# Performance work log

Hardware: AMD Instinct MI355X
Metric: run time of the kernel (lower is better)

The kernel has to match this reference:

```python
import jax, jax.numpy as jnp
import numpy as np

V, E, IN, OUT, K, NREL = 50000, 640000, 128, 128, 4, 237
D = IN // K   # 32
OD = OUT // K # 32

def setup_inputs() -> dict:
    key = jax.random.key(0)
    ks = jax.random.split(key, 20)
    s = 0.05
    return {
        'node_repr': jax.random.normal(ks[0], (V, IN), jnp.float32),
        'rel_repr': jax.random.normal(ks[1], (2 * NREL, IN), jnp.float32),
        'src': jax.random.randint(ks[2], (E,), 0, V, jnp.int32),
        'dst': jax.random.randint(ks[3], (E,), 0, V, jnp.int32),
        'etype': jax.random.randint(ks[4], (E,), 0, 2 * NREL, jnp.int32),
        'norm': jax.random.uniform(ks[5], (E,), jnp.float32),
        'node_w': jax.random.normal(ks[6], (K, IN, D), jnp.float32) * s,
        'node_rel_w': jax.random.normal(ks[7], (K, IN, D), jnp.float32) * s,
        'in_w': jax.random.normal(ks[8], (K, D, OD), jnp.float32) * s,
        'out_w': jax.random.normal(ks[9], (K, D, OD), jnp.float32) * s,
        'att_w': jax.random.normal(ks[10], (2 * D, 1), jnp.float32) * s,
        'loop_rel': jax.random.normal(ks[11], (1, IN), jnp.float32) * s,
        'loop_w': jax.random.normal(ks[12], (IN, OUT), jnp.float32) * s,
        'w_rel': jax.random.normal(ks[13], (IN, OUT), jnp.float32) * s,
        'bias': jnp.zeros((OUT,), jnp.float32),
        'bn_gamma': jnp.ones((OUT,), jnp.float32),
        'bn_beta': jnp.zeros((OUT,), jnp.float32),
    }

def reference(node_repr, rel_repr, src, dst, etype, norm,
              node_w, node_rel_w, in_w, out_w, att_w,
              loop_rel, loop_w, w_rel, bias, bn_gamma, bn_beta):
    e = E
    half = e // 2
    rel = rel_repr  # no bases
    # per-edge composition (opn='mult'): src feature * relation feature
    edge_comp = node_repr[src] * rel[etype]                      # [E, IN]
    edge_data = jnp.einsum('ei,kid->ekd', edge_comp, node_rel_w)  # [E, K, D]
    node_data = jnp.einsum('ei,kid->ekd', node_repr[dst], node_w) # [E, K, D]
    cat = jnp.concatenate([edge_data, node_data], axis=-1)       # [E, K, 2D]
    att = jax.nn.relu(cat @ att_w)                               # [E, K, 1]
    att = jax.nn.softmax(att, axis=1)                            # softmax over K factors
    edge_data = edge_data * att                                  # broadcast over D
    # factorized projection: first half edges -> in_w, second half -> out_w
    msg_in = jnp.einsum('ekd,kdo->eko', edge_data[:half], in_w)
    msg_out = jnp.einsum('ekd,kdo->eko', edge_data[half:], out_w)
    msg = jnp.concatenate([msg_in, msg_out], axis=0).reshape(e, OUT)
    msg = msg * norm[:, None]
    # scatter-sum into destination nodes, then /3 (drop_rate=0)
    h = jax.ops.segment_sum(msg, dst, num_segments=V) / 3.0      # [V, OUT]
    # self-loop term
    h = h + ((h * loop_rel) @ loop_w) / 3.0
    h = h + bias
    # BatchNorm1d (training-mode batch stats, biased variance, eps=1e-5)
    mean = jnp.mean(h, axis=0)
    var = jnp.var(h, axis=0)
    h = bn_gamma * (h - mean) * jax.lax.rsqrt(var + 1e-5) + bn_beta
    node_out = jnp.tanh(h)
    rel_out = rel @ w_rel
    return node_out, rel_out
```

## Files before the change

kernel.cpp:

```cpp
#include <hip/hip_runtime.h>

namespace {
constexpr int V = 50000;
constexpr int E = 640000;
constexpr int HALF = 320000;
constexpr int NREL2 = 474;
constexpr int C = 128;
constexpr int NCHUNK = (V + 255) / 256;
constexpr int NQBLK = V / 16;
constexpr int RELBLK = (NREL2 + 1) / 2;
}

typedef _Float16 h4 __attribute__((ext_vector_type(4)));
typedef _Float16 f16x8 __attribute__((ext_vector_type(8)));
typedef float f32x4 __attribute__((ext_vector_type(4)));

__global__ void prep_kernel(const float* __restrict__ nrw, const float* __restrict__ nw,
                            const float* __restrict__ inw, const float* __restrict__ outw,
                            const float* __restrict__ aw, const float* __restrict__ rel,
                            float* __restrict__ cbuf, float* __restrict__ bbuf,
                            _Float16* __restrict__ Mh, _Float16* __restrict__ rel_h) {
  int tid = blockIdx.x * 256 + threadIdx.x;
  if (tid < 512) {
    int k = tid >> 7, i = tid & 127;
    float acc = 0.f;
    for (int d = 0; d < 32; ++d) acc += nrw[k*4096 + i*32 + d] * aw[d];
    cbuf[tid] = acc;
  } else if (tid < 1024) {
    int u = tid - 512; int k = u >> 7, i = u & 127;
    float acc = 0.f;
    for (int d = 0; d < 32; ++d) acc += nw[k*4096 + i*32 + d] * aw[32 + d];
    bbuf[u] = acc;
  } else if (tid < 1024 + 16384) {
    int u = tid - 1024; int k = u >> 12, rem = u & 4095, i = rem >> 5, o = rem & 31;
    float acc = 0.f;
    for (int d = 0; d < 32; ++d) acc += nrw[k*4096 + i*32 + d] * inw[k*1024 + d*32 + o];
    Mh[(((k) * 2 + (o >> 4)) * 16 + (o & 15)) * 128 + i] = (_Float16)acc;
  } else if (tid < 1024 + 32768) {
    int u = tid - 1024 - 16384; int k = u >> 12, rem = u & 4095, i = rem >> 5, o = rem & 31;
    float acc = 0.f;
    for (int d = 0; d < 32; ++d) acc += nrw[k*4096 + i*32 + d] * outw[k*1024 + d*32 + o];
    Mh[(((4 + k) * 2 + (o >> 4)) * 16 + (o & 15)) * 128 + i] = (_Float16)acc;
  } else if (tid < 1024 + 32768 + NREL2 * C / 8) {
    int u = tid - 1024 - 32768;
    const float4 v0 = *(const float4*)(rel + (size_t)u * 8);
    const float4 v1 = *(const float4*)(rel + (size_t)u * 8 + 4);
    f16x8 o;
    o[0] = (_Float16)v0.x; o[1] = (_Float16)v0.y;
    o[2] = (_Float16)v0.z; o[3] = (_Float16)v0.w;
    o[4] = (_Float16)v1.x; o[5] = (_Float16)v1.y;
    o[6] = (_Float16)v1.z; o[7] = (_Float16)v1.w;
    *(f16x8*)(rel_h + (size_t)u * 8) = o;
  }
}

__global__ __launch_bounds__(256) void qnode_kernel(const float* __restrict__ nrp,
                                                    const float* __restrict__ bbuf,
                                                    float* __restrict__ qbuf,
                                                    _Float16* __restrict__ nrp_h,
                                                    const float* __restrict__ rel,
                                                    const float* __restrict__ wrel,
                                                    float* __restrict__ rel_out) {
  if (blockIdx.x >= NQBLK) {
    __shared__ float rr2[2][128];
    const int bb = blockIdx.x - NQBLK;
    const int half = threadIdx.x >> 7;
    const int t128 = threadIdx.x & 127;
    const int row = bb * 2 + half;
    if (row < NREL2) rr2[half][t128] = rel[row * C + t128];
    __syncthreads();
    if (row < NREL2) {
      float acc = 0.f;
#pragma unroll 4
      for (int i = 0; i < C; ++i) acc += rr2[half][i] * wrel[i * C + t128];
      rel_out[row * C + t128] = acc;
    }
    return;
  }
  const int t = blockIdx.x * 16 + (threadIdx.x >> 4);
  const int l = threadIdx.x & 15;
  if (t >= V) return;
  const float* row = nrp + (size_t)t * C + l * 8;
  float4 a0 = *(const float4*)(row);
  float4 a1 = *(const float4*)(row + 4);
  {
    f16x8 o;
    o[0] = (_Float16)a0.x; o[1] = (_Float16)a0.y;
    o[2] = (_Float16)a0.z; o[3] = (_Float16)a0.w;
    o[4] = (_Float16)a1.x; o[5] = (_Float16)a1.y;
    o[6] = (_Float16)a1.z; o[7] = (_Float16)a1.w;
    *(f16x8*)(nrp_h + (size_t)t * C + l * 8) = o;
  }
  float p[4];
#pragma unroll
  for (int k = 0; k < 4; ++k) {
    const float* brow = bbuf + k * C + l * 8;
    float4 b0 = *(const float4*)(brow);
    float4 b1 = *(const float4*)(brow + 4);
    p[k] = a0.x * b0.x + a0.y * b0.y + a0.z * b0.z + a0.w * b0.w
         + a1.x * b1.x + a1.y * b1.y + a1.z * b1.z + a1.w * b1.w;
  }
#pragma unroll
  for (int m = 1; m < 16; m <<= 1) {
#pragma unroll
    for (int k = 0; k < 4; ++k) p[k] += __shfl_xor(p[k], m);
  }
  if (l == 0) *(float4*)(qbuf + 4 * (size_t)t) = make_float4(p[0], p[1], p[2], p[3]);
}

__global__ void hist_kernel(const int* __restrict__ dst, int* __restrict__ cnt,
                            int* __restrict__ cin) {
  int e = blockIdx.x * 256 + threadIdx.x;
  if (e < E) {
    int t = dst[e];
    atomicAdd(&cnt[t], 1);
    if (e < HALF) atomicAdd(&cin[t], 1);
  }
}

__global__ void scan_sum_kernel(const int* __restrict__ cnt, int* __restrict__ bsum) {
  __shared__ int sd[256];
  int tid = threadIdx.x;
  int idx = blockIdx.x * 256 + tid;
  int v = (idx < V) ? cnt[idx] : 0;
  sd[tid] = v; __syncthreads();
  for (int s = 128; s > 0; s >>= 1) {
    if (tid < s) sd[tid] += sd[tid + s];
    __syncthreads();
  }
  if (tid == 0) bsum[blockIdx.x] = sd[0];
}

__global__ void scan_top_kernel(int* __restrict__ bsum) {
  __shared__ int sd[256];
  int tid = threadIdx.x;
  int v = (tid < NCHUNK) ? bsum[tid] : 0;
  sd[tid] = v; __syncthreads();
  for (int ofs = 1; ofs < 256; ofs <<= 1) {
    int t = (tid >= ofs) ? sd[tid - ofs] : 0;
    __syncthreads();
    sd[tid] += t;
    __syncthreads();
  }
  if (tid < NCHUNK) bsum[tid] = sd[tid] - v;
}

__global__ void scan_apply_kernel(const int* __restrict__ cnt, const int* __restrict__ cin,
                                  const int* __restrict__ bsum, int4* __restrict__ ninfo) {
  __shared__ int sd[256];
  int tid = threadIdx.x;
  int idx = blockIdx.x * 256 + tid;
  int v = (idx < V) ? cnt[idx] : 0;
  sd[tid] = v; __syncthreads();
  for (int ofs = 1; ofs < 256; ofs <<= 1) {
    int t = (tid >= ofs) ? sd[tid - ofs] : 0;
    __syncthreads();
    sd[tid] += t;
    __syncthreads();
  }
  if (idx < V) {
    int off = bsum[blockIdx.x] + sd[tid] - v;
    ninfo[idx] = make_int4(off, v, cin[idx], 0);
  }
}

__global__ void place_kernel(const int* __restrict__ dst, const int* __restrict__ src,
                             const int* __restrict__ etype, const float* __restrict__ norm,
                             const int4* __restrict__ ninfo,
                             int* __restrict__ cur_in, int* __restrict__ cur_out,
                             int2* __restrict__ em) {
  int e = blockIdx.x * 256 + threadIdx.x;
  if (e < E) {
    int t = dst[e];
    int off = ninfo[t].x;
    int pos;
    if (e < HALF) {
      pos = off + atomicAdd(&cur_in[t], 1);
    } else {
      pos = off + ninfo[t].z + atomicAdd(&cur_out[t], 1);
    }
    em[pos] = make_int2(src[e] | (etype[e] << 16), __float_as_int(norm[e]));
  }
}

__global__ __launch_bounds__(256) void fused_kernel(
    const _Float16* __restrict__ nrp_h, const _Float16* __restrict__ rel_h,
    const int4* __restrict__ ninfo, const float* __restrict__ qbuf,
    const float* __restrict__ cbuf, const int2* __restrict__ em,
    const _Float16* __restrict__ Mh, float* __restrict__ h) {
  __shared__ __align__(16) _Float16 z16[16384];
  const int w = threadIdx.x >> 6;
  const int lane = threadIdx.x & 63;
  const int dirg = lane >> 5;
  const int slot = (lane >> 4) & 1;
  const int ll = lane & 15;
  const int ch0 = ll * 8;

  float4 ckA[4], ckB[4];
#pragma unroll
  for (int k = 0; k < 4; ++k) {
    ckA[k] = *(const float4*)(cbuf + k * C + ch0);
    ckB[k] = *(const float4*)(cbuf + k * C + ch0 + 4);
  }

  for (int nn = 0; nn < 4; ++nn) {
    const int node = w * 4 + nn;
    const int t = blockIdx.x * 16 + node;
    const int4 nfo = ninfo[t];
    const int start = nfo.x, deg = nfo.y, ni = nfo.z;
    const float4 q4 = *(const float4*)(qbuf + 4 * (size_t)t);
    const int sidx = dirg ? ni : 0;
    const int nmy = dirg ? (deg - ni) : ni;
    const int nmax = max(ni, deg - ni);

    float4 zA[4], zB[4];
#pragma unroll
    for (int k = 0; k < 4; ++k) {
      zA[k] = make_float4(0.f, 0.f, 0.f, 0.f);
      zB[k] = make_float4(0.f, 0.f, 0.f, 0.f);
    }

    if (nmax > 0) {
      int2 em0 = em[start + min(sidx + slot, deg - 1)];
      int2 em1 = em[start + min(sidx + 2 + slot, deg - 1)];
      f16x8 ah = *(const f16x8*)(nrp_h + (size_t)(em0.x & 0xFFFF) * C + ch0);
      f16x8 bh = *(const f16x8*)(rel_h + (size_t)((em0.x >> 16) & 0x1FF) * C + ch0);

      for (int j = 0; j < nmax; j += 2) {
        int2 em2 = em1;
        if (j + 4 < nmax) em2 = em[start + min(sidx + j + 4 + slot, deg - 1)];
        f16x8 ahn = ah, bhn = bh;
        if (j + 2 < nmax) {
          ahn = *(const f16x8*)(nrp_h + (size_t)(em1.x & 0xFFFF) * C + ch0);
          bhn = *(const f16x8*)(rel_h + (size_t)((em1.x >> 16) & 0x1FF) * C + ch0);
        }
        float4 xA, xB;
        xA.x = (float)ah[0] * (float)bh[0];
        xA.y = (float)ah[1] * (float)bh[1];
        xA.z = (float)ah[2] * (float)bh[2];
        xA.w = (float)ah[3] * (float)bh[3];
        xB.x = (float)ah[4] * (float)bh[4];
        xB.y = (float)ah[5] * (float)bh[5];
        xB.z = (float)ah[6] * (float)bh[6];
        xB.w = (float)ah[7] * (float)bh[7];
        float p0 = xA.x * ckA[0].x + xA.y * ckA[0].y + xA.z * ckA[0].z + xA.w * ckA[0].w
                 + xB.x * ckB[0].x + xB.y * ckB[0].y + xB.z * ckB[0].z + xB.w * ckB[0].w;
        float p1 = xA.x * ckA[1].x + xA.y * ckA[1].y + xA.z * ckA[1].z + xA.w * ckA[1].w
                 + xB.x * ckB[1].x + xB.y * ckB[1].y + xB.z * ckB[1].z + xB.w * ckB[1].w;
        float p2 = xA.x * ckA[2].x + xA.y * ckA[2].y + xA.z * ckA[2].z + xA.w * ckA[2].w
                 + xB.x * ckB[2].x + xB.y * ckB[2].y + xB.z * ckB[2].z + xB.w * ckB[2].w;
        float p3 = xA.x * ckA[3].x + xA.y * ckA[3].y + xA.z * ckA[3].z + xA.w * ckA[3].w
                 + xB.x * ckB[3].x + xB.y * ckB[3].y + xB.z * ckB[3].z + xB.w * ckB[3].w;
#pragma unroll
        for (int m = 1; m < 16; m <<= 1) {
          p0 += __shfl_xor(p0, m);
          p1 += __shfl_xor(p1, m);
          p2 += __shfl_xor(p2, m);
          p3 += __shfl_xor(p3, m);
        }
        float l0 = fmaxf(p0 + q4.x, 0.f);
        float l1 = fmaxf(p1 + q4.y, 0.f);
        float l2 = fmaxf(p2 + q4.z, 0.f);
        float l3 = fmaxf(p3 + q4.w, 0.f);
        float e0f = __expf(l0), e1f = __expf(l1);
        float e2f = __expf(l2), e3f = __expf(l3);
        float nr = __int_as_float(em0.y);
        float inv = ((j + slot) < nmy) ? (nr / (e0f + e1f + e2f + e3f)) : 0.f;
        float w0 = e0f * inv, w1 = e1f * inv, w2 = e2f * inv, w3 = e3f * inv;
        zA[0].x += w0 * xA.x; zA[0].y += w0 * xA.y; zA[0].z += w0 * xA.z; zA[0].w += w0 * xA.w;
        zB[0].x += w0 * xB.x; zB[0].y += w0 * xB.y; zB[0].z += w0 * xB.z; zB[0].w += w0 * xB.w;
        zA[1].x += w1 * xA.x; zA[1].y += w1 * xA.y; zA[1].z += w1 * xA.z; zA[1].w += w1 * xA.w;
        zB[1].x += w1 * xB.x; zB[1].y += w1 * xB.y; zB[1].z += w1 * xB.z; zB[1].w += w1 * xB.w;
        zA[2].x += w2 * xA.x; zA[2].y += w2 * xA.y; zA[2].z += w2 * xA.z; zA[2].w += w2 * xA.w;
        zB[2].x += w2 * xB.x; zB[2].y += w2 * xB.y; zB[2].z += w2 * xB.z; zB[2].w += w2 * xB.w;
        zA[3].x += w3 * xA.x; zA[3].y += w3 * xA.y; zA[3].z += w3 * xA.z; zA[3].w += w3 * xA.w;
        zB[3].x += w3 * xB.x; zB[3].y += w3 * xB.y; zB[3].z += w3 * xB.z; zB[3].w += w3 * xB.w;
        em0 = em1; em1 = em2;
        ah = ahn; bh = bhn;
      }
    }

#pragma unroll
    for (int k = 0; k < 4; ++k) {
      zA[k].x += __shfl_xor(zA[k].x, 16);
      zA[k].y += __shfl_xor(zA[k].y, 16);
      zA[k].z += __shfl_xor(zA[k].z, 16);
      zA[k].w += __shfl_xor(zA[k].w, 16);
      zB[k].x += __shfl_xor(zB[k].x, 16);
      zB[k].y += __shfl_xor(zB[k].y, 16);
      zB[k].z += __shfl_xor(zB[k].z, 16);
      zB[k].w += __shfl_xor(zB[k].w, 16);
    }
    if (slot == 0) {
      const int swz = (node & 7) << 4;
      char* zb = (char*)z16 + node * 2048 + dirg * 1024 + ((ll * 16) ^ swz);
#pragma unroll
      for (int k = 0; k < 4; ++k) {
        f16x8 o;
        o[0] = (_Float16)zA[k].x; o[1] = (_Float16)zA[k].y;
        o[2] = (_Float16)zA[k].z; o[3] = (_Float16)zA[k].w;
        o[4] = (_Float16)zB[k].x; o[5] = (_Float16)zB[k].y;
        o[6] = (_Float16)zB[k].z; o[7] = (_Float16)zB[k].w;
        *(f16x8*)(zb + k * 256) = o;
      }
    }
  }
  __syncthreads();

  const int kk = w;
  const int lo16 = lane & 15;
  const int kq = lane >> 4;
  {
    const int anode = lo16;
    const int aswz = (anode & 7) << 4;
    const char* zb = (const char*)z16 + anode * 2048 + kk * 256;
    f16x8 a[2][4];
#pragma unroll
    for (int d = 0; d < 2; ++d)
#pragma unroll
      for (int kc = 0; kc < 4; ++kc)
        a[d][kc] = *(const f16x8*)(zb + d * 1024 + ((kc * 64 + kq * 16) ^ aswz));

    f32x4 c0 = {0.f, 0.f, 0.f, 0.f};
    f32x4 c1 = {0.f, 0.f, 0.f, 0.f};
#pragma unroll
    for (int d = 0; d < 2; ++d)
#pragma unroll
      for (int kc = 0; kc < 4; ++kc) {
        const _Float16* mb = Mh + (((d * 4 + kk) * 2) * 16 + lo16) * 128 + kc * 32 + kq * 8;
        f16x8 b0 = *(const f16x8*)(mb);
        f16x8 b1 = *(const f16x8*)(mb + 2048);
        c0 = __builtin_amdgcn_mfma_f32_16x16x32_f16(a[d][kc], b0, c0, 0, 0, 0);
        c1 = __builtin_amdgcn_mfma_f32_16x16x32_f16(a[d][kc], b1, c1, 0, 0, 0);
      }

    const float third = 1.f / 3.f;
#pragma unroll
    for (int r = 0; r < 4; ++r) {
      int tt = blockIdx.x * 16 + kq * 4 + r;
      if (tt < V) {
        size_t hb = (size_t)tt * C + kk * 32 + lo16;
        h[hb] = c0[r] * third;
        h[hb + 16] = c1[r] * third;
      }
    }
  }
}

__global__ __launch_bounds__(256, 4) void selfloop_kernel(
    float* __restrict__ h, const float* __restrict__ lr,
    const float* __restrict__ lw, const float* __restrict__ bias,
    float* __restrict__ bnsum, float* __restrict__ bnsq) {
  __shared__ float xr[4][8][128];
  __shared__ float red[256];
  const int tid = threadIdx.x;
  const int w = tid >> 6, lane = tid & 63;

  const int c0 = 2 * lane, c1 = c0 + 1;
  const float lr0 = lr[c0], lr1 = lr[c1];
  const float bv0 = bias[c0], bv1 = bias[c1];
  float s0 = 0.f, s1 = 0.f, sq0 = 0.f, sq1 = 0.f;

  const int wg = blockIdx.x * 4 + w;
  const int nw = gridDim.x * 4;
  for (int rb = wg * 8; rb < V; rb += nw * 8) {
    const int nrows = min(8, V - rb);
    float2 hv[8];
#pragma unroll
    for (int rr = 0; rr < 8; ++rr) {
      if (rr < nrows) {
        hv[rr] = *(const float2*)(h + (size_t)(rb + rr) * C + c0);
      } else {
        hv[rr] = make_float2(0.f, 0.f);
      }
      xr[w][rr][c0] = hv[rr].x * lr0;
      xr[w][rr][c1] = hv[rr].y * lr1;
    }
    float acc[8][2] = {};
    for (int i = 0; i < C; ++i) {
      float2 lwv = *(const float2*)(lw + i * C + c0);
#pragma unroll
      for (int rr = 0; rr < 8; ++rr) {
        float xv = xr[w][rr][i];
        acc[rr][0] += xv * lwv.x;
        acc[rr][1] += xv * lwv.y;
      }
    }
    const float third = 1.f / 3.f;
#pragma unroll
    for (int rr = 0; rr < 8; ++rr) {
      if (rr < nrows) {
        float h0 = hv[rr].x + acc[rr][0] * third + bv0;
        float h1 = hv[rr].y + acc[rr][1] * third + bv1;
        *(float2*)(h + (size_t)(rb + rr) * C + c0) = make_float2(h0, h1);
        s0 += h0; s1 += h1; sq0 += h0 * h0; sq1 += h1 * h1;
      }
    }
  }

  __syncthreads();
  red[tid] = s0; __syncthreads();
  if (tid < 64) {
    float v = red[tid] + red[tid + 64] + red[tid + 128] + red[tid + 192];
    atomicAdd(&bnsum[2 * tid], v);
  }
  __syncthreads();
  red[tid] = s1; __syncthreads();
  if (tid < 64) {
    float v = red[tid] + red[tid + 64] + red[tid + 128] + red[tid + 192];
    atomicAdd(&bnsum[2 * tid + 1], v);
  }
  __syncthreads();
  red[tid] = sq0; __syncthreads();
  if (tid < 64) {
    float v = red[tid] + red[tid + 64] + red[tid + 128] + red[tid + 192];
    atomicAdd(&bnsq[2 * tid], v);
  }
  __syncthreads();
  red[tid] = sq1; __syncthreads();
  if (tid < 64) {
    float v = red[tid] + red[tid + 64] + red[tid + 128] + red[tid + 192];
    atomicAdd(&bnsq[2 * tid + 1], v);
  }
}

__global__ void tanh_kernel(float* __restrict__ h,
                            const float* __restrict__ bnsum, const float* __restrict__ bnsq,
                            const float* __restrict__ gamma, const float* __restrict__ beta) {
  int idx = blockIdx.x * 256 + threadIdx.x;
  int base = idx * 4;
  if (base >= V * C) return;
  int j = base & 127;
  const float invV = 1.f / (float)V;
  float4 v = *(float4*)(h + base);
  float o[4] = {v.x, v.y, v.z, v.w};
#pragma unroll
  for (int cidx = 0; cidx < 4; ++cidx) {
    float mean = bnsum[j + cidx] * invV;
    float var = bnsq[j + cidx] * invV - mean * mean;
    float sc = gamma[j + cidx] * rsqrtf(var + 1e-5f);
    float sh = beta[j + cidx] - sc * mean;
    o[cidx] = tanhf(sc * o[cidx] + sh);
  }
  v.x = o[0]; v.y = o[1]; v.z = o[2]; v.w = o[3];
  *(float4*)(h + base) = v;
}

extern "C" void kernel_launch(void* const* d_in, const int* in_sizes, int n_in,
                              void* d_out, int out_size, void* d_ws, size_t ws_size,
                              hipStream_t stream) {
  const float* node_repr  = (const float*)d_in[0];
  const float* rel_repr   = (const float*)d_in[1];
  const int*   src        = (const int*)d_in[2];
  const int*   dst        = (const int*)d_in[3];
  const int*   etype      = (const int*)d_in[4];
  const float* norm       = (const float*)d_in[5];
  const float* node_w     = (const float*)d_in[6];
  const float* node_rel_w = (const float*)d_in[7];
  const float* in_w       = (const float*)d_in[8];
  const float* out_w      = (const float*)d_in[9];
  const float* att_w      = (const float*)d_in[10];
  const float* loop_rel   = (const float*)d_in[11];
  const float* loop_w     = (const float*)d_in[12];
  const float* w_rel      = (const float*)d_in[13];
  const float* bias       = (const float*)d_in[14];
  const float* bn_gamma   = (const float*)d_in[15];
  const float* bn_beta    = (const float*)d_in[16];

  float* out = (float*)d_out;
  float* h = out;
  float* rel_out = out + (size_t)V * C;

  int* cnt = (int*)d_ws;
  int* cur_in = cnt + V;
  int* cin = cur_in + V;
  int* cur_out = cin + V;
  float* bnsum = (float*)(cur_out + V);
  float* bnsq = bnsum + 128;
  int* bsum = (int*)(bnsq + 128);
  int4* ninfo = (int4*)(bsum + 256);
  int2* em = (int2*)(ninfo + V);
  float* qbuf = (float*)(em + E);
  float* cbuf = qbuf + 4 * V;
  float* bbuf = cbuf + 512;
  _Float16* Mh = (_Float16*)(bbuf + 512);
  _Float16* nrp_h = Mh + 32768;
  _Float16* rel_h = nrp_h + (size_t)V * C;

  hipMemsetAsync(cnt, 0, (size_t)(4 * V + 256) * 4, stream);

  prep_kernel<<<(1024 + 32768 + NREL2 * C / 8 + 255) / 256, 256, 0, stream>>>(
      node_rel_w, node_w, in_w, out_w, att_w, rel_repr, cbuf, bbuf, Mh, rel_h);
  qnode_kernel<<<NQBLK + RELBLK, 256, 0, stream>>>(node_repr, bbuf, qbuf, nrp_h,
                                                   rel_repr, w_rel, rel_out);
  hist_kernel<<<E / 256, 256, 0, stream>>>(dst, cnt, cin);
  scan_sum_kernel<<<NCHUNK, 256, 0, stream>>>(cnt, bsum);
  scan_top_kernel<<<1, 256, 0, stream>>>(bsum);
  scan_apply_kernel<<<NCHUNK, 256, 0, stream>>>(cnt, cin, bsum, ninfo);
  place_kernel<<<E / 256, 256, 0, stream>>>(dst, src, etype, norm, ninfo,
                                            cur_in, cur_out, em);
  fused_kernel<<<(V + 15) / 16, 256, 0, stream>>>(nrp_h, rel_h, ninfo,
                                                  qbuf, cbuf, em, Mh, h);
  selfloop_kernel<<<1024, 256, 0, stream>>>(h, loop_rel, loop_w, bias, bnsum, bnsq);
  tanh_kernel<<<(V * C / 4 + 255) / 256, 256, 0, stream>>>(h, bnsum, bnsq, bn_gamma, bn_beta);
}
```

Measured before the change: 319.2 us.

## Compute self-loop projection with fp16 MFMA using prefolded loop weight matrix

The self-loop GEMM (h*loop_rel)@loop_w/3 moves from a scalar FP32 FMA loop to 16x16x32 fp16 MFMA tiles. loop_rel and the 1/3 factor are folded into a transposed fp16 weight matrix in the prep kernel. Each block stages a 16-row tile of h as fp16 in swizzled shared memory, and the BN partial sums are reduced with wave shuffles instead of shared-memory rounds. The aim is to cut ALU time in this kernel, at the cost of fp16 rounding of h and of the weights in the self-loop term.

Result: faster. 270.2 us (-15.4%).

```diff
diff --git a/kernel.cpp b/kernel.cpp
--- a/kernel.cpp
+++ b/kernel.cpp
@@ -9,6 +9,7 @@
 constexpr int NCHUNK = (V + 255) / 256;
 constexpr int NQBLK = V / 16;
 constexpr int RELBLK = (NREL2 + 1) / 2;
+constexpr int NTILES = V / 16;
 }
 
 typedef _Float16 h4 __attribute__((ext_vector_type(4)));
@@ -18,8 +19,10 @@
 __global__ void prep_kernel(const float* __restrict__ nrw, const float* __restrict__ nw,
                             const float* __restrict__ inw, const float* __restrict__ outw,
                             const float* __restrict__ aw, const float* __restrict__ rel,
+                            const float* __restrict__ lr, const float* __restrict__ lw,
                             float* __restrict__ cbuf, float* __restrict__ bbuf,
-                            _Float16* __restrict__ Mh, _Float16* __restrict__ rel_h) {
+                            _Float16* __restrict__ Mh, _Float16* __restrict__ rel_h,
+                            _Float16* __restrict__ LWh) {
   int tid = blockIdx.x * 256 + threadIdx.x;
   if (tid < 512) {
     int k = tid >> 7, i = tid & 127;
@@ -51,6 +54,11 @@
     o[4] = (_Float16)v1.x; o[5] = (_Float16)v1.y;
     o[6] = (_Float16)v1.z; o[7] = (_Float16)v1.w;
     *(f16x8*)(rel_h + (size_t)u * 8) = o;
+  } else if (tid < 1024 + 32768 + NREL2 * C / 8 + 16384) {
+    int u = tid - 1024 - 32768 - NREL2 * C / 8;
+    int o = u >> 7, i = u & 127;
+    float v = lr[i] * lw[i * C + o] * (1.f / 3.f);
+    LWh[u] = (_Float16)v;
   }
 }
 
@@ -347,80 +355,73 @@
   }
 }
 
-__global__ __launch_bounds__(256, 4) void selfloop_kernel(
-    float* __restrict__ h, const float* __restrict__ lr,
-    const float* __restrict__ lw, const float* __restrict__ bias,
+__global__ __launch_bounds__(256) void selfloop_kernel(
+    float* __restrict__ h, const _Float16* __restrict__ LWh,
+    const float* __restrict__ bias,
     float* __restrict__ bnsum, float* __restrict__ bnsq) {
-  __shared__ float xr[4][8][128];
-  __shared__ float red[256];
+  __shared__ __align__(16) _Float16 hf[2048];
   const int tid = threadIdx.x;
   const int w = tid >> 6, lane = tid & 63;
-
-  const int c0 = 2 * lane, c1 = c0 + 1;
-  const float lr0 = lr[c0], lr1 = lr[c1];
-  const float bv0 = bias[c0], bv1 = bias[c1];
+  const int row = tid >> 4;
+  const int l = tid & 15;
+  const int lo16 = lane & 15;
+  const int kq = lane >> 4;
+  const float bv0 = bias[w * 32 + lo16];
+  const float bv1 = bias[w * 32 + 16 + lo16];
   float s0 = 0.f, s1 = 0.f, sq0 = 0.f, sq1 = 0.f;
 
-  const int wg = blockIdx.x * 4 + w;
-  const int nw = gridDim.x * 4;
-  for (int rb = wg * 8; rb < V; rb += nw * 8) {
-    const int nrows = min(8, V - rb);
-    float2 hv[8];
-#pragma unroll
-    for (int rr = 0; rr < 8; ++rr) {
-      if (rr < nrows) {
-        hv[rr] = *(const float2*)(h + (size_t)(rb + rr) * C + c0);
-      } else {
-        hv[rr] = make_float2(0.f, 0.f);
-      }
-      xr[w][rr][c0] = hv[rr].x * lr0;
-      xr[w][rr][c1] = hv[rr].y * lr1;
-    }
-    float acc[8][2] = {};
-    for (int i = 0; i < C; ++i) {
-      float2 lwv = *(const float2*)(lw + i * C + c0);
-#pragma unroll
-      for (int rr = 0; rr < 8; ++rr) {
-        float xv = xr[w][rr][i];
-        acc[rr][0] += xv * lwv.x;
-        acc[rr][1] += xv * lwv.y;
-      }
-    }
-    const float third = 1.f / 3.f;
-#pragma unroll
-    for (int rr = 0; rr < 8; ++rr) {
-      if (rr < nrows) {
-        float h0 = hv[rr].x + acc[rr][0] * third + bv0;
-        float h1 = hv[rr].y + acc[rr][1] * third + bv1;
-        *(float2*)(h + (size_t)(rb + rr) * C + c0) = make_float2(h0, h1);
-        s0 += h0; s1 += h1; sq0 += h0 * h0; sq1 += h1 * h1;
-      }
-    }
-  }
-
-  __syncthreads();
-  red[tid] = s0; __syncthreads();
-  if (tid < 64) {
-    float v = red[tid] + red[tid + 64] + red[tid + 128] + red[tid + 192];
-    atomicAdd(&bnsum[2 * tid], v);
-  }
-  __syncthreads();
-  red[tid] = s1; __syncthreads();
-  if (tid < 64) {
-    float v = red[tid] + red[tid + 64] + red[tid + 128] + red[tid + 192];
-    atomicAdd(&bnsum[2 * tid + 1], v);
-  }
-  __syncthreads();
-  red[tid] = sq0; __syncthreads();
-  if (tid < 64) {
-    float v = red[tid] + red[tid + 64] + red[tid + 128] + red[tid + 192];
-    atomicAdd(&bnsq[2 * tid], v);
-  }
-  __syncthreads();
-  red[tid] = sq1; __syncthreads();
-  if (tid < 64) {
-    float v = red[tid] + red[tid + 64] + red[tid + 128] + red[tid + 192];
-    atomicAdd(&bnsq[2 * tid + 1], v);
+  const int aswz = (lo16 & 7) << 4;
+  const int lswz = (row & 7) << 4;
+
+  for (int tile = blockIdx.x; tile < NTILES; tile += gridDim.x) {
+    {
+      const float* hp = h + (size_t)(tile * 16 + row) * C + l * 8;
+      float4 v0 = *(const float4*)(hp);
+      float4 v1 = *(const float4*)(hp + 4);
+      f16x8 o;
+      o[0] = (_Float16)v0.x; o[1] = (_Float16)v0.y;
+      o[2] = (_Float16)v0.z; o[3] = (_Float16)v0.w;
+      o[4] = (_Float16)v1.x; o[5] = (_Float16)v1.y;
+      o[6] = (_Float16)v1.z; o[7] = (_Float16)v1.w;
+      *(f16x8*)((char*)hf + row * 256 + ((l * 16) ^ lswz)) = o;
+    }
+    __syncthreads();
+
+    const char* zb = (const char*)hf + lo16 * 256;
+    f32x4 c0 = {0.f, 0.f, 0.f, 0.f};
+    f32x4 c1 = {0.f, 0.f, 0.f, 0.f};
+#pragma unroll
+    for (int kc = 0; kc < 4; ++kc) {
+      f16x8 a = *(const f16x8*)(zb + ((kc * 64 + kq * 16) ^ aswz));
+      const _Float16* mb = LWh + ((w * 2) * 16 + lo16) * 128 + kc * 32 + kq * 8;
+      f16x8 b0 = *(const f16x8*)(mb);
+      f16x8 b1 = *(const f16x8*)(mb + 2048);
+      c0 = __builtin_amdgcn_mfma_f32_16x16x32_f16(a, b0, c0, 0, 0, 0);
+      c1 = __builtin_amdgcn_mfma_f32_16x16x32_f16(a, b1, c1, 0, 0, 0);
+    }
+
+#pragma unroll
+    for (int r = 0; r < 4; ++r) {
+      int tt = tile * 16 + kq * 4 + r;
+      size_t hb = (size_t)tt * C + w * 32 + lo16;
+      float h0 = h[hb] + c0[r] + bv0;
+      float h1 = h[hb + 16] + c1[r] + bv1;
+      h[hb] = h0;
+      h[hb + 16] = h1;
+      s0 += h0; s1 += h1; sq0 += h0 * h0; sq1 += h1 * h1;
+    }
+    __syncthreads();
+  }
+
+  s0 += __shfl_xor(s0, 16); s0 += __shfl_xor(s0, 32);
+  s1 += __shfl_xor(s1, 16); s1 += __shfl_xor(s1, 32);
+  sq0 += __shfl_xor(sq0, 16); sq0 += __shfl_xor(sq0, 32);
+  sq1 += __shfl_xor(sq1, 16); sq1 += __shfl_xor(sq1, 32);
+  if (kq == 0) {
+    atomicAdd(&bnsum[w * 32 + lo16], s0);
+    atomicAdd(&bnsum[w * 32 + 16 + lo16], s1);
+    atomicAdd(&bnsq[w * 32 + lo16], sq0);
+    atomicAdd(&bnsq[w * 32 + 16 + lo16], sq1);
   }
 }
 
@@ -484,13 +485,15 @@
   float* cbuf = qbuf + 4 * V;
   float* bbuf = cbuf + 512;
   _Float16* Mh = (_Float16*)(bbuf + 512);
-  _Float16* nrp_h = Mh + 32768;
+  _Float16* LWh = Mh + 32768;
+  _Float16* nrp_h = LWh + 16384;
   _Float16* rel_h = nrp_h + (size_t)V * C;
 
   hipMemsetAsync(cnt, 0, (size_t)(4 * V + 256) * 4, stream);
 
-  prep_kernel<<<(1024 + 32768 + NREL2 * C / 8 + 255) / 256, 256, 0, stream>>>(
-      node_rel_w, node_w, in_w, out_w, att_w, rel_repr, cbuf, bbuf, Mh, rel_h);
+  prep_kernel<<<(1024 + 32768 + NREL2 * C / 8 + 16384 + 255) / 256, 256, 0, stream>>>(
+      node_rel_w, node_w, in_w, out_w, att_w, rel_repr, loop_rel, loop_w,
+      cbuf, bbuf, Mh, rel_h, LWh);
   qnode_kernel<<<NQBLK + RELBLK, 256, 0, stream>>>(node_repr, bbuf, qbuf, nrp_h,
                                                    rel_repr, w_rel, rel_out);
   hist_kernel<<<E / 256, 256, 0, stream>>>(dst, cnt, cin);
@@ -501,6 +504,6 @@
                                             cur_in, cur_out, em);
   fused_kernel<<<(V + 15) / 16, 256, 0, stream>>>(nrp_h, rel_h, ninfo,
                                                   qbuf, cbuf, em, Mh, h);
-  selfloop_kernel<<<1024, 256, 0, stream>>>(h, loop_rel, loop_w, bias, bnsum, bnsq);
+  selfloop_kernel<<<640, 256, 0, stream>>>(h, LWh, bias, bnsum, bnsq);
   tanh_kernel<<<(V * C / 4 + 255) / 256, 256, 0, stream>>>(h, bnsum, bnsq, bn_gamma, bn_beta);
 }
```
